# Kernel tuning notes

Hardware: AMD Instinct MI355X
Metric: run time of the kernel (lower is better)

The kernel has to match this reference:

```python
import jax, jax.numpy as jnp
import numpy as np

N_NODES = 100000
NEG_SLOPE = 0.2


def gat_layer(x, src, dst, W, al, ar, b):
    # x: [N, F_in]; src/dst: [E]; W: [F_in, F_out]; al/ar/b: [F_out]
    h = x @ W                                  # [N, F_out]
    el = h @ al                                # [N] per-src attention term
    er = h @ ar                                # [N] per-dst attention term
    e = jax.nn.leaky_relu(el[src] + er[dst], NEG_SLOPE)   # [E]
    # edge softmax over incoming edges of each dst node (numerically stable)
    mx = jax.ops.segment_max(e, dst, num_segments=N_NODES)
    mx = jnp.where(jnp.isfinite(mx), mx, 0.0)  # zero-in-degree guard
    ex = jnp.exp(e - mx[dst])
    denom = jax.ops.segment_sum(ex, dst, num_segments=N_NODES)
    alpha = ex / jnp.maximum(denom[dst], 1e-9)             # [E]
    out = jax.ops.segment_sum(alpha[:, None] * h[src], dst, num_segments=N_NODES)
    return out + b


def setup_inputs() -> dict:
    key = jax.random.key(0)
    ks = jax.random.split(key, 11)
    N, E, F_in, F_h = N_NODES, 1600000, 128, 64
    x = jax.random.normal(ks[0], (N, F_in), dtype=jnp.float32)
    src = jax.random.randint(ks[1], (E,), 0, N, dtype=jnp.int32)
    dst = jax.random.randint(ks[2], (E,), 0, N, dtype=jnp.int32)
    s1 = 1.0 / np.sqrt(F_in)
    s2 = 1.0 / np.sqrt(F_h)
    W1 = jax.random.normal(ks[3], (F_in, F_h), dtype=jnp.float32) * s1
    al1 = jax.random.normal(ks[4], (F_h,), dtype=jnp.float32) * s2
    ar1 = jax.random.normal(ks[5], (F_h,), dtype=jnp.float32) * s2
    b1 = jnp.zeros((F_h,), dtype=jnp.float32)
    W2 = jax.random.normal(ks[6], (F_h, F_h), dtype=jnp.float32) * s2
    al2 = jax.random.normal(ks[7], (F_h,), dtype=jnp.float32) * s2
    ar2 = jax.random.normal(ks[8], (F_h,), dtype=jnp.float32) * s2
    b2 = jnp.zeros((F_h,), dtype=jnp.float32)
    return {"x": x, "src": src, "dst": dst, "W1": W1, "al1": al1, "ar1": ar1,
            "b1": b1, "W2": W2, "al2": al2, "ar2": ar2, "b2": b2}


def reference(x, src, dst, W1, al1, ar1, b1, W2, al2, ar2, b2):
    h = gat_layer(x, src, dst, W1, al1, ar1, b1)   # conv1, head squeezed
    h = jax.nn.relu(h)                              # dropout = identity (eval)
    h = gat_layer(h, src, dst, W2, al2, ar2, b2)   # conv2
    return h
```

## Files before the change

### kernel.cpp

```cpp
#include <hip/hip_runtime.h>
#include <hip/hip_fp16.h>

#define NNODES 100000
#define NEG_SLOPE 0.2f
#define NBK 49
#define BKSHIFT 11
#define BKMASK 2047
#define BCAP 35328
#define B1 4096
#define SLSTRIDE 56

typedef _Float16 f16x8 __attribute__((ext_vector_type(8)));
typedef float f32x4 __attribute__((ext_vector_type(4)));


__global__ void k_init(int* __restrict__ gcur, int* __restrict__ offs, int N, int E) {
    int t = threadIdx.x;
    if (t < NBK) gcur[t] = t * BCAP;
    if (t == NBK) offs[N] = E;
}


__global__ __launch_bounds__(256, 4) void k_gemm1b(
    const float* __restrict__ x, const float* __restrict__ W,
    const float* __restrict__ al, const float* __restrict__ ar,
    __half* __restrict__ h, float* __restrict__ el, float* __restrict__ er,
    int N, int nbBin,
    const int* __restrict__ src, const int* __restrict__ dst,
    int* __restrict__ gcur, int* __restrict__ be, int E) {

    __shared__ float4 SMEM[2048];
    __shared__ int lcnt[NBK], lbase[NBK], lcur[NBK];
    int t = threadIdx.x;

    if ((int)blockIdx.x < nbBin) {
        int base = (int)blockIdx.x * B1;
        if (t < NBK) lcnt[t] = 0;
        __syncthreads();
        int dreg[16];
#pragma unroll
        for (int j = 0; j < 16; ++j) {
            int e = base + j * 256 + t;
            dreg[j] = (e < E) ? dst[e] : -1;
            if (e < E) atomicAdd(&lcnt[dreg[j] >> BKSHIFT], 1);
        }
        __syncthreads();
        if (t < NBK) { lbase[t] = atomicAdd(&gcur[t], lcnt[t]); lcur[t] = 0; }
        __syncthreads();
#pragma unroll
        for (int j = 0; j < 16; ++j) {
            int e = base + j * 256 + t;
            if (e < E) {
                int d = dreg[j];
                int bk = d >> BKSHIFT;
                int p = lbase[bk] + atomicAdd(&lcur[bk], 1);
                be[p] = (src[e] << BKSHIFT) | (d & BKMASK);
            }
        }
        return;
    }

    char* A  = (char*)SMEM;
    char* Bw = (char*)SMEM + 16384;
    int row0 = ((int)blockIdx.x - nbBin) * 64;

    for (int i = t; i < 2048; i += 256) {
        int r = i >> 5, c4 = i & 31;
        int rr = row0 + r; if (rr > N - 1) rr = N - 1;
        float4 v = *(const float4*)(x + (size_t)rr * 128 + c4 * 4);
        int byte = r * 256 + ((c4 * 8) ^ ((r & 7) << 4));
        *(__half2*)(A + byte)     = __floats2half2_rn(v.x, v.y);
        *(__half2*)(A + byte + 4) = __floats2half2_rn(v.z, v.w);
    }
    for (int i = t; i < 2048; i += 256) {
        int k = i >> 4, c4 = (i & 15) * 4;
        float4 v = *(const float4*)(W + k * 64 + c4);
        int kb = k * 2;
        *(__half*)(Bw + (c4 + 0) * 256 + (kb ^ (((c4 + 0) & 7) << 4))) = __float2half(v.x);
        *(__half*)(Bw + (c4 + 1) * 256 + (kb ^ (((c4 + 1) & 7) << 4))) = __float2half(v.y);
        *(__half*)(Bw + (c4 + 2) * 256 + (kb ^ (((c4 + 2) & 7) << 4))) = __float2half(v.z);
        *(__half*)(Bw + (c4 + 3) * 256 + (kb ^ (((c4 + 3) & 7) << 4))) = __float2half(v.w);
    }
    __syncthreads();

    int w = t >> 6, l = t & 63, g = l >> 4, c = l & 15;
    int swz = (c & 7) << 4;
    const char* Ar = A + (w * 16 + c) * 256;

    f32x4 acc[4];
#pragma unroll
    for (int t2 = 0; t2 < 4; ++t2) acc[t2] = (f32x4){0.f, 0.f, 0.f, 0.f};
#pragma unroll
    for (int kk = 0; kk < 4; ++kk) {
        int kb = kk * 64 + g * 16;
        f16x8 av = *(const f16x8*)(Ar + (kb ^ swz));
#pragma unroll
        for (int t2 = 0; t2 < 4; ++t2) {
            f16x8 bv = *(const f16x8*)(Bw + (t2 * 16 + c) * 256 + (kb ^ swz));
            acc[t2] = __builtin_amdgcn_mfma_f32_16x16x32_f16(av, bv, acc[t2], 0, 0, 0);
        }
    }

    float alv[4], arv[4];
#pragma unroll
    for (int t2 = 0; t2 < 4; ++t2) { alv[t2] = al[t2 * 16 + c]; arv[t2] = ar[t2 * 16 + c]; }
#pragma unroll
    for (int r = 0; r < 4; ++r) {
        float e1 = 0.f, e2 = 0.f;
#pragma unroll
        for (int t2 = 0; t2 < 4; ++t2) {
            e1 = fmaf(acc[t2][r], alv[t2], e1);
            e2 = fmaf(acc[t2][r], arv[t2], e2);
        }
#pragma unroll
        for (int o = 1; o < 16; o <<= 1) { e1 += __shfl_xor(e1, o); e2 += __shfl_xor(e2, o); }
        int row = row0 + w * 16 + 4 * g + r;
        if (row < N) {
            if (c == 0) { el[row] = e1; er[row] = e2; }
#pragma unroll
            for (int t2 = 0; t2 < 4; ++t2)
                h[(size_t)row * 64 + t2 * 16 + c] = __float2half(acc[t2][r]);
        }
    }
}


__global__ __launch_bounds__(256) void k_offs(const int* __restrict__ be,
                                              const int* __restrict__ gcur,
                                              int* __restrict__ offs, int N) {
    __shared__ int cnt[2048];
    __shared__ int sb[2][256];
    __shared__ int rbeg;
    int B = blockIdx.x, t = threadIdx.x;
    int mycnt = gcur[B] - B * BCAP;
    int ebase = B * BCAP;

    for (int i = t; i < 2048; i += 256) cnt[i] = 0;
    if (t == 0) rbeg = 0;
    __syncthreads();
    for (int i = t; i < mycnt; i += 256) atomicAdd(&cnt[be[ebase + i] & BKMASK], 1);
    if (t < 64) {
        int v = (t < B) ? gcur[t] - t * BCAP : 0;
#pragma unroll
        for (int o = 32; o; o >>= 1) v += __shfl_xor(v, o);
        if (t == 0) rbeg = v;
    }
    __syncthreads();

    int loc[8], s = 0;
#pragma unroll
    for (int i = 0; i < 8; ++i) { loc[i] = s; s += cnt[8 * t + i]; }
    sb[0][t] = s;
    __syncthreads();
    int pi = 0;
    for (int d = 1; d < 256; d <<= 1) {
        int po = pi ^ 1;
        sb[po][t] = sb[pi][t] + (t >= d ? sb[pi][t - d] : 0);
        pi = po;
        __syncthreads();
    }
    int bas = rbeg + sb[pi][t] - s;

    int node0 = (B << BKSHIFT) + 8 * t;
#pragma unroll
    for (int i = 0; i < 8; ++i) {
        int node = node0 + i;
        if (node < N) offs[node] = bas + loc[i];
    }
}


__global__ __launch_bounds__(256) void k_scat(const int* __restrict__ be,
                                              const int* __restrict__ gcur,
                                              const int* __restrict__ offs,
                                              int* __restrict__ csr, int N) {
    int b = blockIdx.x;
    int B = b % SLSTRIDE, sl = b / SLSTRIDE;
    if (B >= NBK) return;

    __shared__ int cur[256];
    int t = threadIdx.x;
    int mycnt = gcur[B] - B * BCAP;
    int ebase = B * BCAP;
    int node = (B << BKSHIFT) + sl * 256 + t;
    cur[t] = (node < N) ? offs[node] : 0;
    __syncthreads();
    for (int i = t; i < mycnt; i += 256) {
        int v = be[ebase + i];
        int loc = v & BKMASK;
        if ((loc >> 8) == sl) {
            int p = atomicAdd(&cur[loc & 255], 1);
            csr[p] = v >> BKSHIFT;
        }
    }
}


__global__ __launch_bounds__(256, 4) void k_gemm2(
    const __half* __restrict__ xin, const float* __restrict__ W,
    const float* __restrict__ al, const float* __restrict__ ar,
    __half* __restrict__ h, float* __restrict__ el, float* __restrict__ er, int N) {

    __shared__ float4 AlR[512];
    __shared__ float4 WtR[512];
    char* A = (char*)AlR;
    char* Bw = (char*)WtR;
    int tid = threadIdx.x;
    int row0 = blockIdx.x * 64;

    for (int i = tid; i < 512; i += 256) {
        int r = i >> 3, o = i & 7;
        int rr = row0 + r; if (rr > N - 1) rr = N - 1;
        float4 v = *(const float4*)(xin + (size_t)rr * 64 + o * 8);
        *(float4*)(A + r * 128 + ((o * 16) ^ ((r & 7) << 4))) = v;
    }
    for (int i = tid; i < 1024; i += 256) {
        int k = i >> 4, c4 = (i & 15) * 4;
        float4 v = *(const float4*)(W + k * 64 + c4);
        int kb = k * 2;
        *(__half*)(Bw + (c4 + 0) * 128 + (kb ^ (((c4 + 0) & 7) << 4))) = __float2half(v.x);
        *(__half*)(Bw + (c4 + 1) * 128 + (kb ^ (((c4 + 1) & 7) << 4))) = __float2half(v.y);
        *(__half*)(Bw + (c4 + 2) * 128 + (kb ^ (((c4 + 2) & 7) << 4))) = __float2half(v.z);
        *(__half*)(Bw + (c4 + 3) * 128 + (kb ^ (((c4 + 3) & 7) << 4))) = __float2half(v.w);
    }
    __syncthreads();

    int w = tid >> 6, l = tid & 63, g = l >> 4, c = l & 15;
    int swz = (c & 7) << 4;
    const char* Ar = A + (w * 16 + c) * 128;

    f32x4 acc[4];
#pragma unroll
    for (int t2 = 0; t2 < 4; ++t2) acc[t2] = (f32x4){0.f, 0.f, 0.f, 0.f};
#pragma unroll
    for (int kk = 0; kk < 2; ++kk) {
        int kb = kk * 64 + g * 16;
        f16x8 av = *(const f16x8*)(Ar + (kb ^ swz));
#pragma unroll
        for (int t2 = 0; t2 < 4; ++t2) {
            f16x8 bv = *(const f16x8*)(Bw + (t2 * 16 + c) * 128 + (kb ^ swz));
            acc[t2] = __builtin_amdgcn_mfma_f32_16x16x32_f16(av, bv, acc[t2], 0, 0, 0);
        }
    }

    float alv[4], arv[4];
#pragma unroll
    for (int t2 = 0; t2 < 4; ++t2) { alv[t2] = al[t2 * 16 + c]; arv[t2] = ar[t2 * 16 + c]; }
#pragma unroll
    for (int r = 0; r < 4; ++r) {
        float e1 = 0.f, e2 = 0.f;
#pragma unroll
        for (int t2 = 0; t2 < 4; ++t2) {
            e1 = fmaf(acc[t2][r], alv[t2], e1);
            e2 = fmaf(acc[t2][r], arv[t2], e2);
        }
#pragma unroll
        for (int o = 1; o < 16; o <<= 1) { e1 += __shfl_xor(e1, o); e2 += __shfl_xor(e2, o); }
        int row = row0 + w * 16 + 4 * g + r;
        if (row < N) {
            if (c == 0) { el[row] = e1; er[row] = e2; }
#pragma unroll
            for (int t2 = 0; t2 < 4; ++t2)
                h[(size_t)row * 64 + t2 * 16 + c] = __float2half(acc[t2][r]);
        }
    }
}


__device__ inline float2 h2_to_f2(float bits) {
    return __half22float2(__builtin_bit_cast(__half2, bits));
}

template <bool OUT_HALF>
__global__ __launch_bounds__(256) void k_agg(const __half* __restrict__ h,
                                             const float* __restrict__ el,
                                             const float* __restrict__ er,
                                             const float* __restrict__ b,
                                             const int* __restrict__ offs,
                                             const int* __restrict__ csr_src,
                                             void* __restrict__ outp, int N, int relu) {
    int wave = threadIdx.x >> 6, lane = threadIdx.x & 63;
    int n = blockIdx.x * 4 + wave;
    if (n >= N) return;

    int beg = offs[n], end = offs[n + 1];
    int deg = end - beg;
    float ern = er[n];

    int g = lane >> 4;
    int fl = lane & 15;
    float4 accv = make_float4(0.f, 0.f, 0.f, 0.f);
    const size_t foff = 4 * (size_t)fl;

    if (deg <= 64) {
        int sidx = 0;
        float e = -1e30f;
        if (lane < deg) {
            sidx = csr_src[beg + lane];
            e = el[sidx] + ern;
            e = e > 0.f ? e : NEG_SLOPE * e;
        }
        float m = e;
#pragma unroll
        for (int o = 32; o; o >>= 1) m = fmaxf(m, __shfl_xor(m, o));
        float p = (lane < deg) ? __expf(e - m) : 0.f;
        float s = p;
#pragma unroll
        for (int o = 32; o; o >>= 1) s += __shfl_xor(s, o);
        float a = p * (1.f / fmaxf(s, 1e-9f));

        int iters = (deg + 3) >> 2;
        int quad = iters >> 2;
        int i = g;
        for (int t4 = 0; t4 < quad; ++t4, i += 16) {
            int s0 = __shfl(sidx, i),     s1 = __shfl(sidx, i + 4);
            int s2 = __shfl(sidx, i + 8), s3 = __shfl(sidx, i + 12);
            float w0 = __shfl(a, i),     w1 = __shfl(a, i + 4);
            float w2 = __shfl(a, i + 8), w3 = __shfl(a, i + 12);
            float2 r0 = *(const float2*)(h + (size_t)s0 * 64 + foff);
            float2 r1 = *(const float2*)(h + (size_t)s1 * 64 + foff);
            float2 r2 = *(const float2*)(h + (size_t)s2 * 64 + foff);
            float2 r3 = *(const float2*)(h + (size_t)s3 * 64 + foff);
            float2 f00 = h2_to_f2(r0.x), f01 = h2_to_f2(r0.y);
            float2 f10 = h2_to_f2(r1.x), f11 = h2_to_f2(r1.y);
            float2 f20 = h2_to_f2(r2.x), f21 = h2_to_f2(r2.y);
            float2 f30 = h2_to_f2(r3.x), f31 = h2_to_f2(r3.y);
            accv.x = fmaf(w0, f00.x, accv.x); accv.y = fmaf(w0, f00.y, accv.y);
            accv.z = fmaf(w0, f01.x, accv.z); accv.w = fmaf(w0, f01.y, accv.w);
            accv.x = fmaf(w1, f10.x, accv.x); accv.y = fmaf(w1, f10.y, accv.y);
            accv.z = fmaf(w1, f11.x, accv.z); accv.w = fmaf(w1, f11.y, accv.w);
            accv.x = fmaf(w2, f20.x, accv.x); accv.y = fmaf(w2, f20.y, accv.y);
            accv.z = fmaf(w2, f21.x, accv.z); accv.w = fmaf(w2, f21.y, accv.w);
            accv.x = fmaf(w3, f30.x, accv.x); accv.y = fmaf(w3, f30.y, accv.y);
            accv.z = fmaf(w3, f31.x, accv.z); accv.w = fmaf(w3, f31.y, accv.w);
        }
        int rem = iters & 3;
        for (int rr2 = 0; rr2 < rem; ++rr2, i += 4) {
            int s0 = __shfl(sidx, i);
            float w0 = __shfl(a, i);
            float2 r0 = *(const float2*)(h + (size_t)s0 * 64 + foff);
            float2 f00 = h2_to_f2(r0.x), f01 = h2_to_f2(r0.y);
            accv.x = fmaf(w0, f00.x, accv.x); accv.y = fmaf(w0, f00.y, accv.y);
            accv.z = fmaf(w0, f01.x, accv.z); accv.w = fmaf(w0, f01.y, accv.w);
        }
    } else {
        float m = -1e30f;
        for (int i = beg + lane; i < end; i += 64) {
            float e = el[csr_src[i]] + ern;
            e = e > 0.f ? e : NEG_SLOPE * e;
            m = fmaxf(m, e);
        }
#pragma unroll
        for (int o = 32; o; o >>= 1) m = fmaxf(m, __shfl_xor(m, o));
        float s = 0.f;
        for (int i = beg + lane; i < end; i += 64) {
            float e = el[csr_src[i]] + ern;
            e = e > 0.f ? e : NEG_SLOPE * e;
            s += __expf(e - m);
        }
#pragma unroll
        for (int o = 32; o; o >>= 1) s += __shfl_xor(s, o);
        float inv = 1.f / fmaxf(s, 1e-9f);

        for (int i = g; i < deg; i += 4) {
            int s0 = csr_src[beg + i];
            float e = el[s0] + ern;
            e = e > 0.f ? e : NEG_SLOPE * e;
            float w0 = __expf(e - m) * inv;
            float2 r0 = *(const float2*)(h + (size_t)s0 * 64 + foff);
            float2 f00 = h2_to_f2(r0.x), f01 = h2_to_f2(r0.y);
            accv.x = fmaf(w0, f00.x, accv.x); accv.y = fmaf(w0, f00.y, accv.y);
            accv.z = fmaf(w0, f01.x, accv.z); accv.w = fmaf(w0, f01.y, accv.w);
        }
    }

#pragma unroll
    for (int o = 16; o <= 32; o <<= 1) {
        accv.x += __shfl_xor(accv.x, o);
        accv.y += __shfl_xor(accv.y, o);
        accv.z += __shfl_xor(accv.z, o);
        accv.w += __shfl_xor(accv.w, o);
    }

    if (lane < 16) {
        float4 bv = *(const float4*)(b + foff);
        float ox = accv.x + bv.x, oy = accv.y + bv.y;
        float oz = accv.z + bv.z, ow = accv.w + bv.w;
        if (relu) {
            ox = fmaxf(ox, 0.f); oy = fmaxf(oy, 0.f);
            oz = fmaxf(oz, 0.f); ow = fmaxf(ow, 0.f);
        }
        if (OUT_HALF) {
            __half* oh = (__half*)outp + (size_t)n * 64 + foff;
            *(__half2*)(oh)     = __floats2half2_rn(ox, oy);
            *(__half2*)(oh + 2) = __floats2half2_rn(oz, ow);
        } else {
            *(float4*)((float*)outp + (size_t)n * 64 + foff) = make_float4(ox, oy, oz, ow);
        }
    }
}


extern "C" void kernel_launch(void* const* d_in, const int* in_sizes, int n_in,
                              void* d_out, int out_size, void* d_ws, size_t ws_size,
                              hipStream_t stream) {
    const float* x   = (const float*)d_in[0];
    const int*   src = (const int*)d_in[1];
    const int*   dst = (const int*)d_in[2];
    const float* W1  = (const float*)d_in[3];
    const float* al1 = (const float*)d_in[4];
    const float* ar1 = (const float*)d_in[5];
    const float* b1  = (const float*)d_in[6];
    const float* W2  = (const float*)d_in[7];
    const float* al2 = (const float*)d_in[8];
    const float* ar2 = (const float*)d_in[9];
    const float* b2  = (const float*)d_in[10];
    float* out = (float*)d_out;

    const int N = NNODES;
    const int E = in_sizes[1];

    __half* h    = (__half*)d_ws;
    __half* hmid = h + (size_t)N * 64;
    int*    be   = (int*)(hmid + (size_t)N * 64);
    int*    csr  = be + (size_t)NBK * BCAP;
    float*  el   = (float*)(csr + E);
    float*  er   = el + N;
    int*    offs = (int*)(er + N);
    int*    gcur = offs + N + 1;

    int nbBin = (E + B1 - 1) / B1;
    int nbG   = (N + 63) / 64;
    int nbR   = (N + 3) / 4;

    k_init<<<1, 64, 0, stream>>>(gcur, offs, N, E);
    k_gemm1b<<<nbBin + nbG, 256, 0, stream>>>(x, W1, al1, ar1, h, el, er, N,
                                              nbBin, src, dst, gcur, be, E);
    k_offs<<<NBK, 256, 0, stream>>>(be, gcur, offs, N);
    k_scat<<<8 * SLSTRIDE, 256, 0, stream>>>(be, gcur, offs, csr, N);
    k_agg<true><<<nbR, 256, 0, stream>>>(h, el, er, b1, offs, csr, hmid, N, 1);
    k_gemm2<<<nbG, 256, 0, stream>>>(hmid, W2, al2, ar2, h, el, er, N);
    k_agg<false><<<nbR, 256, 0, stream>>>(h, el, er, b2, offs, csr, out, N, 0);
}
```

Baseline: 211.1 us.

## Fuse layer-1 aggregation with layer-2 GEMM through shared memory

The layer-1 edge-softmax aggregation and the layer-2 projection GEMM now run in one kernel. Each block aggregates 64 nodes, one per wave for 16 iterations, and writes the ReLU'd fp16 result straight into swizzled LDS. It then runs the MFMA GEMM and attention dot products from there, which removes the hmid round trip through global memory and one launch. The cost is fewer, larger blocks with serial per-wave node loops, which may reduce latency hiding for the irregular gathers; separate el2/er2 buffers are added so layer-1 data is not overwritten while still being read.

```diff
diff --git a/kernel.cpp b/kernel.cpp
--- a/kernel.cpp
+++ b/kernel.cpp
@@ -196,101 +196,15 @@
 }
 
 
-__global__ __launch_bounds__(256, 4) void k_gemm2(
-    const __half* __restrict__ xin, const float* __restrict__ W,
-    const float* __restrict__ al, const float* __restrict__ ar,
-    __half* __restrict__ h, float* __restrict__ el, float* __restrict__ er, int N) {
-
-    __shared__ float4 AlR[512];
-    __shared__ float4 WtR[512];
-    char* A = (char*)AlR;
-    char* Bw = (char*)WtR;
-    int tid = threadIdx.x;
-    int row0 = blockIdx.x * 64;
-
-    for (int i = tid; i < 512; i += 256) {
-        int r = i >> 3, o = i & 7;
-        int rr = row0 + r; if (rr > N - 1) rr = N - 1;
-        float4 v = *(const float4*)(xin + (size_t)rr * 64 + o * 8);
-        *(float4*)(A + r * 128 + ((o * 16) ^ ((r & 7) << 4))) = v;
-    }
-    for (int i = tid; i < 1024; i += 256) {
-        int k = i >> 4, c4 = (i & 15) * 4;
-        float4 v = *(const float4*)(W + k * 64 + c4);
-        int kb = k * 2;
-        *(__half*)(Bw + (c4 + 0) * 128 + (kb ^ (((c4 + 0) & 7) << 4))) = __float2half(v.x);
-        *(__half*)(Bw + (c4 + 1) * 128 + (kb ^ (((c4 + 1) & 7) << 4))) = __float2half(v.y);
-        *(__half*)(Bw + (c4 + 2) * 128 + (kb ^ (((c4 + 2) & 7) << 4))) = __float2half(v.z);
-        *(__half*)(Bw + (c4 + 3) * 128 + (kb ^ (((c4 + 3) & 7) << 4))) = __float2half(v.w);
-    }
-    __syncthreads();
-
-    int w = tid >> 6, l = tid & 63, g = l >> 4, c = l & 15;
-    int swz = (c & 7) << 4;
-    const char* Ar = A + (w * 16 + c) * 128;
-
-    f32x4 acc[4];
-#pragma unroll
-    for (int t2 = 0; t2 < 4; ++t2) acc[t2] = (f32x4){0.f, 0.f, 0.f, 0.f};
-#pragma unroll
-    for (int kk = 0; kk < 2; ++kk) {
-        int kb = kk * 64 + g * 16;
-        f16x8 av = *(const f16x8*)(Ar + (kb ^ swz));
-#pragma unroll
-        for (int t2 = 0; t2 < 4; ++t2) {
-            f16x8 bv = *(const f16x8*)(Bw + (t2 * 16 + c) * 128 + (kb ^ swz));
-            acc[t2] = __builtin_amdgcn_mfma_f32_16x16x32_f16(av, bv, acc[t2], 0, 0, 0);
-        }
-    }
-
-    float alv[4], arv[4];
-#pragma unroll
-    for (int t2 = 0; t2 < 4; ++t2) { alv[t2] = al[t2 * 16 + c]; arv[t2] = ar[t2 * 16 + c]; }
-#pragma unroll
-    for (int r = 0; r < 4; ++r) {
-        float e1 = 0.f, e2 = 0.f;
-#pragma unroll
-        for (int t2 = 0; t2 < 4; ++t2) {
-            e1 = fmaf(acc[t2][r], alv[t2], e1);
-            e2 = fmaf(acc[t2][r], arv[t2], e2);
-        }
-#pragma unroll
-        for (int o = 1; o < 16; o <<= 1) { e1 += __shfl_xor(e1, o); e2 += __shfl_xor(e2, o); }
-        int row = row0 + w * 16 + 4 * g + r;
-        if (row < N) {
-            if (c == 0) { el[row] = e1; er[row] = e2; }
-#pragma unroll
-            for (int t2 = 0; t2 < 4; ++t2)
-                h[(size_t)row * 64 + t2 * 16 + c] = __float2half(acc[t2][r]);
-        }
-    }
-}
-
-
 __device__ inline float2 h2_to_f2(float bits) {
     return __half22float2(__builtin_bit_cast(__half2, bits));
 }
 
-template <bool OUT_HALF>
-__global__ __launch_bounds__(256) void k_agg(const __half* __restrict__ h,
-                                             const float* __restrict__ el,
-                                             const float* __restrict__ er,
-                                             const float* __restrict__ b,
-                                             const int* __restrict__ offs,
-                                             const int* __restrict__ csr_src,
-                                             void* __restrict__ outp, int N, int relu) {
-    int wave = threadIdx.x >> 6, lane = threadIdx.x & 63;
-    int n = blockIdx.x * 4 + wave;
-    if (n >= N) return;
-
-    int beg = offs[n], end = offs[n + 1];
-    int deg = end - beg;
-    float ern = er[n];
-
-    int g = lane >> 4;
-    int fl = lane & 15;
+__device__ float4 agg_node(const __half* __restrict__ h,
+                           const float* __restrict__ el, float ern,
+                           const int* __restrict__ csr_src,
+                           int beg, int deg, int lane, int g, size_t foff) {
     float4 accv = make_float4(0.f, 0.f, 0.f, 0.f);
-    const size_t foff = 4 * (size_t)fl;
 
     if (deg <= 64) {
         int sidx = 0;
@@ -344,6 +258,7 @@
             accv.z = fmaf(w0, f01.x, accv.z); accv.w = fmaf(w0, f01.y, accv.w);
         }
     } else {
+        int end = beg + deg;
         float m = -1e30f;
         for (int i = beg + lane; i < end; i += 64) {
             float e = el[csr_src[i]] + ern;
@@ -361,7 +276,6 @@
 #pragma unroll
         for (int o = 32; o; o >>= 1) s += __shfl_xor(s, o);
         float inv = 1.f / fmaxf(s, 1e-9f);
-
         for (int i = g; i < deg; i += 4) {
             int s0 = csr_src[beg + i];
             float e = el[s0] + ern;
@@ -381,22 +295,127 @@
         accv.z += __shfl_xor(accv.z, o);
         accv.w += __shfl_xor(accv.w, o);
     }
+    return accv;
+}
+
+
+__global__ __launch_bounds__(256, 4) void k_aggemm(
+    const __half* __restrict__ h, const float* __restrict__ el,
+    const float* __restrict__ er, const float* __restrict__ b1,
+    const int* __restrict__ offs, const int* __restrict__ csr_src,
+    const float* __restrict__ W2, const float* __restrict__ al2,
+    const float* __restrict__ ar2,
+    __half* __restrict__ h2, float* __restrict__ el2, float* __restrict__ er2,
+    int N) {
+
+    __shared__ float4 SMEM[1024];
+    char* A  = (char*)SMEM;
+    char* Bw = (char*)SMEM + 8192;
+    int t = threadIdx.x;
+    int w = t >> 6, lane = t & 63, g = lane >> 4, fl = lane & 15;
+    int row0 = blockIdx.x * 64;
+
+    for (int i = t; i < 1024; i += 256) {
+        int k = i >> 4, c4 = (i & 15) * 4;
+        float4 v = *(const float4*)(W2 + k * 64 + c4);
+        int kb = k * 2;
+        *(__half*)(Bw + (c4 + 0) * 128 + (kb ^ (((c4 + 0) & 7) << 4))) = __float2half(v.x);
+        *(__half*)(Bw + (c4 + 1) * 128 + (kb ^ (((c4 + 1) & 7) << 4))) = __float2half(v.y);
+        *(__half*)(Bw + (c4 + 2) * 128 + (kb ^ (((c4 + 2) & 7) << 4))) = __float2half(v.z);
+        *(__half*)(Bw + (c4 + 3) * 128 + (kb ^ (((c4 + 3) & 7) << 4))) = __float2half(v.w);
+    }
+
+    const size_t foff = 4 * (size_t)fl;
+    float4 bv = *(const float4*)(b1 + foff);
+    for (int j = 0; j < 16; ++j) {
+        int r = w * 16 + j;
+        int n = row0 + r;
+        int beg = 0, deg = 0;
+        float ern = 0.f;
+        if (n < N) {
+            beg = offs[n];
+            deg = offs[n + 1] - beg;
+            ern = er[n];
+        }
+        float4 accv = agg_node(h, el, ern, csr_src, beg, deg, lane, g, foff);
+        if (lane < 16) {
+            float ox = fmaxf(accv.x + bv.x, 0.f);
+            float oy = fmaxf(accv.y + bv.y, 0.f);
+            float oz = fmaxf(accv.z + bv.z, 0.f);
+            float ow = fmaxf(accv.w + bv.w, 0.f);
+            __half2 h01 = __floats2half2_rn(ox, oy);
+            __half2 h23 = __floats2half2_rn(oz, ow);
+            float2 pk;
+            pk.x = __builtin_bit_cast(float, h01);
+            pk.y = __builtin_bit_cast(float, h23);
+            *(float2*)(A + r * 128 + ((int)(fl * 8) ^ ((r & 7) << 4))) = pk;
+        }
+    }
+    __syncthreads();
+
+    int c = fl;
+    int swz = (c & 7) << 4;
+    const char* Ar = A + (w * 16 + c) * 128;
+
+    f32x4 acc[4];
+#pragma unroll
+    for (int t2 = 0; t2 < 4; ++t2) acc[t2] = (f32x4){0.f, 0.f, 0.f, 0.f};
+#pragma unroll
+    for (int kk = 0; kk < 2; ++kk) {
+        int kb = kk * 64 + g * 16;
+        f16x8 av = *(const f16x8*)(Ar + (kb ^ swz));
+#pragma unroll
+        for (int t2 = 0; t2 < 4; ++t2) {
+            f16x8 bvf = *(const f16x8*)(Bw + (t2 * 16 + c) * 128 + (kb ^ swz));
+            acc[t2] = __builtin_amdgcn_mfma_f32_16x16x32_f16(av, bvf, acc[t2], 0, 0, 0);
+        }
+    }
+
+    float alv[4], arv[4];
+#pragma unroll
+    for (int t2 = 0; t2 < 4; ++t2) { alv[t2] = al2[t2 * 16 + c]; arv[t2] = ar2[t2 * 16 + c]; }
+#pragma unroll
+    for (int r = 0; r < 4; ++r) {
+        float e1 = 0.f, e2 = 0.f;
+#pragma unroll
+        for (int t2 = 0; t2 < 4; ++t2) {
+            e1 = fmaf(acc[t2][r], alv[t2], e1);
+            e2 = fmaf(acc[t2][r], arv[t2], e2);
+        }
+#pragma unroll
+        for (int o = 1; o < 16; o <<= 1) { e1 += __shfl_xor(e1, o); e2 += __shfl_xor(e2, o); }
+        int row = row0 + w * 16 + 4 * g + r;
+        if (row < N) {
+            if (c == 0) { el2[row] = e1; er2[row] = e2; }
+#pragma unroll
+            for (int t2 = 0; t2 < 4; ++t2)
+                h2[(size_t)row * 64 + t2 * 16 + c] = __float2half(acc[t2][r]);
+        }
+    }
+}
+
+
+__global__ __launch_bounds__(256) void k_agg2(const __half* __restrict__ h,
+                                              const float* __restrict__ el,
+                                              const float* __restrict__ er,
+                                              const float* __restrict__ b,
+                                              const int* __restrict__ offs,
+                                              const int* __restrict__ csr_src,
+                                              float* __restrict__ out, int N) {
+    int wave = threadIdx.x >> 6, lane = threadIdx.x & 63;
+    int n = blockIdx.x * 4 + wave;
+    if (n >= N) return;
+
+    int beg = offs[n], deg = offs[n + 1] - beg;
+    int g = lane >> 4, fl = lane & 15;
+    const size_t foff = 4 * (size_t)fl;
+
+    float4 accv = agg_node(h, el, er[n], csr_src, beg, deg, lane, g, foff);
 
     if (lane < 16) {
         float4 bv = *(const float4*)(b + foff);
-        float ox = accv.x + bv.x, oy = accv.y + bv.y;
-        float oz = accv.z + bv.z, ow = accv.w + bv.w;
-        if (relu) {
-            ox = fmaxf(ox, 0.f); oy = fmaxf(oy, 0.f);
-            oz = fmaxf(oz, 0.f); ow = fmaxf(ow, 0.f);
-        }
-        if (OUT_HALF) {
-            __half* oh = (__half*)outp + (size_t)n * 64 + foff;
-            *(__half2*)(oh)     = __floats2half2_rn(ox, oy);
-            *(__half2*)(oh + 2) = __floats2half2_rn(oz, ow);
-        } else {
-            *(float4*)((float*)outp + (size_t)n * 64 + foff) = make_float4(ox, oy, oz, ow);
-        }
+        *(float4*)(out + (size_t)n * 64 + foff) =
+            make_float4(accv.x + bv.x, accv.y + bv.y, accv.z + bv.z, accv.w + bv.w);
     }
 }
 
@@ -421,12 +440,14 @@
     const int E = in_sizes[1];
 
     __half* h    = (__half*)d_ws;
-    __half* hmid = h + (size_t)N * 64;
-    int*    be   = (int*)(hmid + (size_t)N * 64);
+    __half* h2   = h + (size_t)N * 64;
+    int*    be   = (int*)(h2 + (size_t)N * 64);
     int*    csr  = be + (size_t)NBK * BCAP;
     float*  el   = (float*)(csr + E);
     float*  er   = el + N;
-    int*    offs = (int*)(er + N);
+    float*  el2  = er + N;
+    float*  er2  = el2 + N;
+    int*    offs = (int*)(er2 + N);
     int*    gcur = offs + N + 1;
 
     int nbBin = (E + B1 - 1) / B1;
@@ -438,7 +459,7 @@
                                               nbBin, src, dst, gcur, be, E);
     k_offs<<<NBK, 256, 0, stream>>>(be, gcur, offs, N);
     k_scat<<<8 * SLSTRIDE, 256, 0, stream>>>(be, gcur, offs, csr, N);
-    k_agg<true><<<nbR, 256, 0, stream>>>(h, el, er, b1, offs, csr, hmid, N, 1);
-    k_gemm2<<<nbG, 256, 0, stream>>>(hmid, W2, al2, ar2, h, el, er, N);
-    k_agg<false><<<nbR, 256, 0, stream>>>(h, el, er, b2, offs, csr, out, N, 0);
-}
+    k_aggemm<<<nbG, 256, 0, stream>>>(h, el, er, b1, offs, csr,
+                                      W2, al2, ar2, h2, el2, er2, N);
+    k_agg2<<<nbR, 256, 0, stream>>>(h2, el2, er2, b2, offs, csr, out, N);
+}
```

After: 203.2 us. -3.8%, faster.
